# Kernel tuning notes

Hardware: AMD Instinct MI355X
Metric: run time of the kernel (lower is better)

## Reference

```python
import jax, jax.numpy as jnp
import numpy as np

N = 512          # nodes per sample (num_nodes)
B = 8            # batch size (samples)
H = 64           # hidden_dim
SPARSITY = 0.1
K = int(SPARSITY * N * (N - 1))  # edges kept per sample (fixed, static)


def setup_inputs() -> dict:
    key = jax.random.key(0)
    ks = jax.random.split(key, 8)

    def lin(k, fi, fo):
        w = jax.random.normal(k, (fi, fo), jnp.float32) / np.sqrt(fi).astype(np.float32)
        b = jnp.zeros((fo,), jnp.float32)
        return w, b

    w_emb, b_emb = lin(ks[0], 1, H)
    w_proj, b_proj = lin(ks[1], H, H)
    w1, b1 = lin(ks[2], 2 * H, H)
    w2, b2 = lin(ks[3], H, H // 2)
    w3, b3 = lin(ks[4], H // 2, 1)
    x = jax.random.uniform(ks[5], (B * N, 1), jnp.float32)  # abundances >= 0
    batch = jnp.repeat(jnp.arange(B, dtype=jnp.int32), N)   # [B*N]
    return dict(x=x, w_emb=w_emb, b_emb=b_emb, w_proj=w_proj, b_proj=b_proj,
                w1=w1, b1=b1, w2=w2, b2=b2, w3=w3, b3=b3, batch=batch)


def reference(x, w_emb, b_emb, w_proj, b_proj, w1, b1, w2, b2, w3, b3, batch):
    # node embedding + projection (dropout is eval-mode no-op)
    emb = jax.nn.relu(x @ w_emb + b_emb) @ w_proj + b_proj     # [B*N, H]
    emb = emb.reshape(B, N, H)
    # first pairwise-MLP layer: cat([e_i, e_j]) @ w1 == e_i @ w1a + e_j @ w1b
    w1a, w1b = w1[:H], w1[H:]
    ai = emb @ w1a                                            # [B, N, H]
    aj = emb @ w1b                                            # [B, N, H]
    h1 = jax.nn.relu(ai[:, :, None, :] + aj[:, None, :, :] + b1)   # [B, N, N, H]
    h2 = jax.nn.relu(jnp.einsum('bijh,hk->bijk', h1, w2) + b2)     # [B, N, N, H/2]
    probs = jax.nn.sigmoid(jnp.einsum('bijk,ko->bij', h2, w3) + b3[0])  # [B, N, N]
    probs = 0.5 * (probs + jnp.swapaxes(probs, 1, 2))          # symmetrize
    probs = probs * (1.0 - jnp.eye(N, dtype=probs.dtype))      # mask diagonal
    flat = probs.reshape(B, N * N)
    _, idx = jax.lax.top_k(flat, K)                            # [B, K]
    idx = jnp.sort(idx, axis=-1)                               # row-major order (dense_to_sparse)
    vals = jnp.take_along_axis(flat, idx, axis=-1)             # [B, K]
    offsets = (jnp.arange(B) * N)[:, None]                     # node offset per sample
    rows = idx // N + offsets
    cols = idx % N + offsets
    edge_index = jnp.stack([rows.reshape(-1), cols.reshape(-1)], axis=0)  # [2, B*K]
    edge_weights = vals.reshape(-1)                            # [B*K]
    adj = jnp.zeros((B, N * N), flat.dtype).at[jnp.arange(B)[:, None], idx].set(vals)
    adj = adj.reshape(B, N, N)                                 # sparse adjacency per sample
    return edge_index, edge_weights, adj
```

## Files before the change

kernel.cpp:

```cpp
#include <hip/hip_runtime.h>

#define NV 512
#define BV 8
#define KSEL 26163
#define NNv (NV*NV)
#define BKv (BV*KSEL)
#define CAPB 32768
#define DELTA 1e-4f

typedef unsigned int u32;
typedef __attribute__((ext_vector_type(8))) _Float16 f16x8;
typedef __attribute__((ext_vector_type(4))) float f32x4;

__global__ void __launch_bounds__(256) k_embed(
    const float* __restrict__ x, const float* __restrict__ w_emb,
    const float* __restrict__ b_emb, const float* __restrict__ w_proj,
    const float* __restrict__ b_proj, const float* __restrict__ w1,
    const float* __restrict__ b1,
    float* __restrict__ ai, float* __restrict__ aj, float* __restrict__ ajb) {
    __shared__ float sh[4][64];
    __shared__ float se[4][64];
    const int c = threadIdx.x;
    const int lr = threadIdx.y;
    const int row = blockIdx.x * 4 + lr;
    const float xv = x[row];
    sh[lr][c] = fmaxf(fmaf(xv, w_emb[c], b_emb[c]), 0.f);
    __syncthreads();
    float e = 0.f;
#pragma unroll
    for (int h = 0; h < 64; ++h) e = fmaf(sh[lr][h], w_proj[h * 64 + c], e);
    se[lr][c] = e + b_proj[c];
    __syncthreads();
    float a0 = 0.f, a1 = 0.f;
#pragma unroll
    for (int h = 0; h < 64; ++h) {
        const float ev = se[lr][h];
        a0 = fmaf(ev, w1[h * 64 + c], a0);
        a1 = fmaf(ev, w1[(64 + h) * 64 + c], a1);
    }
    ai[row * 64 + c] = a0;
    aj[row * 64 + c] = a1;
    ajb[row * 64 + c] = a1 + b1[c];
}

__global__ void __launch_bounds__(256) k_pairs_mfma(
    const float* __restrict__ ai, const float* __restrict__ ajb,
    const float* __restrict__ w2, const float* __restrict__ b2,
    const float* __restrict__ w3, const float* __restrict__ b3,
    float* __restrict__ probs) {
    __shared__ float s_ai[2048];
    const int tid = threadIdx.x;
    const int b = blockIdx.z;
    const int i0 = blockIdx.y << 5;
    const int j0 = blockIdx.x << 6;
    {
        const int r = tid >> 3, c8 = (tid & 7) << 3;
        const float* src = &ai[(((b << 9) + i0 + r) << 6) + c8];
        *(float4*)&s_ai[(r << 6) + c8]     = *(const float4*)&src[0];
        *(float4*)&s_ai[(r << 6) + c8 + 4] = *(const float4*)&src[4];
    }
    const int lane = tid & 63;
    const int wv = tid >> 6;
    const int lp = lane & 15;
    const int lg = lane >> 4;
    const int j = j0 + (wv << 4) + lp;

    float ajr[2][8];
    {
        const float* base = &ajb[(((b << 9) + j) << 6) + (lg << 3)];
        *(float4*)&ajr[0][0] = *(const float4*)&base[0];
        *(float4*)&ajr[0][4] = *(const float4*)&base[4];
        *(float4*)&ajr[1][0] = *(const float4*)&base[32];
        *(float4*)&ajr[1][4] = *(const float4*)&base[36];
    }
    f16x8 Ah[2][2], Al[2][2];
#pragma unroll
    for (int kt = 0; kt < 2; ++kt)
#pragma unroll
        for (int ch = 0; ch < 2; ++ch)
#pragma unroll
            for (int e = 0; e < 8; ++e) {
                const float wv2 = w2[((ch << 5) + (lg << 3) + e) * 32 + (kt << 4) + lp];
                const _Float16 wh = (_Float16)wv2;
                Ah[kt][ch][e] = wh;
                Al[kt][ch][e] = (_Float16)((wv2 - (float)wh) * 2048.0f);
            }
    float b2r[2][4], w3r[2][4];
#pragma unroll
    for (int kt = 0; kt < 2; ++kt)
#pragma unroll
        for (int r = 0; r < 4; ++r) {
            b2r[kt][r] = b2[(kt << 4) + (lg << 2) + r];
            w3r[kt][r] = w3[(kt << 4) + (lg << 2) + r];
        }
    const float b3v = b3[0];
    __syncthreads();

    for (int i = 0; i < 32; ++i) {
        float ar[2][8];
        const float* arow = &s_ai[(i << 6) + (lg << 3)];
        *(float4*)&ar[0][0] = *(const float4*)&arow[0];
        *(float4*)&ar[0][4] = *(const float4*)&arow[4];
        *(float4*)&ar[1][0] = *(const float4*)&arow[32];
        *(float4*)&ar[1][4] = *(const float4*)&arow[36];
        f16x8 Bh0, Bh1, Bl0, Bl1;
#pragma unroll
        for (int e = 0; e < 8; ++e) {
            const float t0 = fmaxf(ar[0][e] + ajr[0][e], 0.f) * 256.0f;
            const float t1 = fmaxf(ar[1][e] + ajr[1][e], 0.f) * 256.0f;
            const _Float16 h0 = (_Float16)t0;
            const _Float16 h1 = (_Float16)t1;
            Bh0[e] = h0; Bl0[e] = (_Float16)((t0 - (float)h0) * 2048.0f);
            Bh1[e] = h1; Bl1[e] = (_Float16)((t1 - (float)h1) * 2048.0f);
        }
        f32x4 am0 = {0.f,0.f,0.f,0.f}, am1 = {0.f,0.f,0.f,0.f};
        f32x4 ac0 = {0.f,0.f,0.f,0.f}, ac1 = {0.f,0.f,0.f,0.f};
        am0 = __builtin_amdgcn_mfma_f32_16x16x32_f16(Ah[0][0], Bh0, am0, 0, 0, 0);
        am0 = __builtin_amdgcn_mfma_f32_16x16x32_f16(Ah[0][1], Bh1, am0, 0, 0, 0);
        ac0 = __builtin_amdgcn_mfma_f32_16x16x32_f16(Ah[0][0], Bl0, ac0, 0, 0, 0);
        ac0 = __builtin_amdgcn_mfma_f32_16x16x32_f16(Ah[0][1], Bl1, ac0, 0, 0, 0);
        ac0 = __builtin_amdgcn_mfma_f32_16x16x32_f16(Al[0][0], Bh0, ac0, 0, 0, 0);
        ac0 = __builtin_amdgcn_mfma_f32_16x16x32_f16(Al[0][1], Bh1, ac0, 0, 0, 0);
        am1 = __builtin_amdgcn_mfma_f32_16x16x32_f16(Ah[1][0], Bh0, am1, 0, 0, 0);
        am1 = __builtin_amdgcn_mfma_f32_16x16x32_f16(Ah[1][1], Bh1, am1, 0, 0, 0);
        ac1 = __builtin_amdgcn_mfma_f32_16x16x32_f16(Ah[1][0], Bl0, ac1, 0, 0, 0);
        ac1 = __builtin_amdgcn_mfma_f32_16x16x32_f16(Ah[1][1], Bl1, ac1, 0, 0, 0);
        ac1 = __builtin_amdgcn_mfma_f32_16x16x32_f16(Al[1][0], Bh0, ac1, 0, 0, 0);
        ac1 = __builtin_amdgcn_mfma_f32_16x16x32_f16(Al[1][1], Bh1, ac1, 0, 0, 0);
        float s = 0.f;
#pragma unroll
        for (int r = 0; r < 4; ++r) {
            const float h2 = fmaf(ac0[r], 1.9073486328125e-6f, am0[r] * 0.00390625f);
            s = fmaf(fmaxf(h2 + b2r[0][r], 0.f), w3r[0][r], s);
        }
#pragma unroll
        for (int r = 0; r < 4; ++r) {
            const float h2 = fmaf(ac1[r], 1.9073486328125e-6f, am1[r] * 0.00390625f);
            s = fmaf(fmaxf(h2 + b2r[1][r], 0.f), w3r[1][r], s);
        }
        s += __shfl_xor(s, 16);
        s += __shfl_xor(s, 32);
        const float p = 1.f / (1.f + expf(-(s + b3v)));
        if (lane < 16) probs[(((b << 9) + i0 + i) << 9) + j] = p;
    }
}

__global__ void k_sym(float* __restrict__ P) {
    const int b = blockIdx.y;
    int rem = blockIdx.x, ta = 0;
    while (rem >= 16 - ta) { rem -= 16 - ta; ++ta; }
    const int tb = ta + rem;
    const int r  = threadIdx.x >> 3;
    const int c4 = (threadIdx.x & 7) << 2;
    const int i = (ta << 5) + r;
    const int j = (tb << 5) + c4;
    float* Pb = P + b * NNv;
    float4 a = *(const float4*)&Pb[(i << 9) + j];
    float t0 = Pb[((j + 0) << 9) + i];
    float t1 = Pb[((j + 1) << 9) + i];
    float t2 = Pb[((j + 2) << 9) + i];
    float t3 = Pb[((j + 3) << 9) + i];
    __syncthreads();
    float4 o;
    o.x = (i == j + 0) ? 0.f : 0.5f * (a.x + t0);
    o.y = (i == j + 1) ? 0.f : 0.5f * (a.y + t1);
    o.z = (i == j + 2) ? 0.f : 0.5f * (a.z + t2);
    o.w = (i == j + 3) ? 0.f : 0.5f * (a.w + t3);
    *(float4*)&Pb[(i << 9) + j] = o;
    Pb[((j + 0) << 9) + i] = o.x;
    Pb[((j + 1) << 9) + i] = o.y;
    Pb[((j + 2) << 9) + i] = o.z;
    Pb[((j + 3) << 9) + i] = o.w;
}

template <int PASS>
__global__ void k_hist(const float* __restrict__ probs,
                       const u32* __restrict__ prefix, u32* __restrict__ hist) {
    __shared__ u32 lh[1024];
    const int t = threadIdx.x;
    lh[t] = 0u; lh[256 + t] = 0u; lh[512 + t] = 0u; lh[768 + t] = 0u;
    __syncthreads();
    const int b = blockIdx.y;
    u32 pref = 0u;
    if constexpr (PASS > 0) pref = prefix[b];
    const float* Pb = probs + b * NNv;
    const int base = blockIdx.x * 4096 + t;
    const int rep = (t & 3) << 8;
#pragma unroll
    for (int e = 0; e < 16; ++e) {
        const u32 key = __float_as_uint(Pb[base + e * 256]);
        bool ok = true;
        if constexpr (PASS > 0) ok = ((key >> (32 - 8 * PASS)) == pref);
        if (ok) atomicAdd(&lh[rep + ((key >> (24 - 8 * PASS)) & 255u)], 1u);
    }
    __syncthreads();
    const u32 sum = lh[t] + lh[256 + t] + lh[512 + t] + lh[768 + t];
    if (sum) atomicAdd(&hist[b * 256 + t], sum);
}

template <int FIRST>
__global__ void k_selp(const u32* __restrict__ hist, u32* __restrict__ prefix,
                       u32* __restrict__ rem) {
    __shared__ u32 s[256];
    const int b = blockIdx.x, t = threadIdx.x;
    s[t] = hist[b * 256 + t];
    __syncthreads();
    for (int off = 1; off < 256; off <<= 1) {
        const u32 v = (t + off < 256) ? s[t + off] : 0u;
        __syncthreads();
        s[t] += v;
        __syncthreads();
    }
    const u32 remv = FIRST ? (u32)KSEL : rem[b];
    const u32 above = (t < 255) ? s[t + 1] : 0u;
    if (s[t] >= remv && above < remv) {
        rem[b] = remv - above;
        prefix[b] = (prefix[b] << 8) | (u32)t;
    }
}

__global__ void k_thr(const u32* __restrict__ prefix, float* __restrict__ thr) {
    const int b = threadIdx.x;
    if (b >= 8) return;
    const u32 p24 = prefix[b];
    thr[b]     = __uint_as_float(p24 << 8) - 2.f * DELTA;
    thr[8 + b] = __uint_as_float((p24 + 1u) << 8) + 2.f * DELTA;
}

__global__ void __launch_bounds__(256) k_band(
    const float* __restrict__ P, const float* __restrict__ thr,
    u32* __restrict__ C_in, u32* __restrict__ bandCnt, u32* __restrict__ bandIdx) {
    __shared__ u32 lidx[1024];
    __shared__ u32 lcnt, lhi, gbase;
    const int b = blockIdx.y, blk = blockIdx.x, t = threadIdx.x;
    if (t == 0) { lcnt = 0u; lhi = 0u; }
    __syncthreads();
    const float Tlo = thr[b], Thi = thr[8 + b];
    const int fi0 = blk * 1024 + t * 4;
    const float4 v = *(const float4*)&P[b * NNv + fi0];
    const float vv[4] = {v.x, v.y, v.z, v.w};
    u32 hc = 0;
#pragma unroll
    for (int q = 0; q < 4; ++q) {
        const float xq = vv[q];
        if (xq > Thi) ++hc;
        else if (xq >= Tlo) { u32 p = atomicAdd(&lcnt, 1u); lidx[p] = (u32)(fi0 + q); }
    }
    if (hc) atomicAdd(&lhi, hc);
    __syncthreads();
    if (t == 0) {
        if (lhi) atomicAdd(&C_in[b], lhi);
        gbase = lcnt ? atomicAdd(&bandCnt[b], lcnt) : 0u;
    }
    __syncthreads();
    for (u32 p = t; p < lcnt; p += 256) {
        const u32 g = gbase + p;
        if (g < (u32)CAPB) bandIdx[b * CAPB + g] = lidx[p];
    }
}

__device__ __forceinline__ float exact_p(const float* __restrict__ rai,
                                         const float* __restrict__ raj,
                                         const float* __restrict__ s_w2,
                                         const float* __restrict__ s_b1,
                                         const float* __restrict__ s_b2,
                                         const float* __restrict__ s_w3,
                                         float b3v) {
    float acc[32];
#pragma unroll
    for (int k = 0; k < 32; ++k) acc[k] = 0.f;
#pragma unroll 1
    for (int h0 = 0; h0 < 64; h0 += 16) {
        float A[16], J[16];
#pragma unroll
        for (int q = 0; q < 4; ++q) {
            *(float4*)&A[q * 4] = *(const float4*)&rai[h0 + q * 4];
            *(float4*)&J[q * 4] = *(const float4*)&raj[h0 + q * 4];
        }
#pragma unroll
        for (int hh = 0; hh < 16; ++hh) {
            const float tv = fmaxf((A[hh] + J[hh]) + s_b1[h0 + hh], 0.f);
#pragma unroll
            for (int k = 0; k < 32; ++k) acc[k] = fmaf(tv, s_w2[(h0 + hh) * 32 + k], acc[k]);
        }
    }
    float d = 0.f;
#pragma unroll
    for (int k = 0; k < 32; ++k) d = fmaf(fmaxf(acc[k] + s_b2[k], 0.f), s_w3[k], d);
    return 1.f / (1.f + expf(-(d + b3v)));
}

__global__ void __launch_bounds__(256) k_band_exact(
    const float* __restrict__ ai, const float* __restrict__ aj,
    const float* __restrict__ b1, const float* __restrict__ w2,
    const float* __restrict__ b2, const float* __restrict__ w3,
    const float* __restrict__ b3, const u32* __restrict__ bandCnt,
    const u32* __restrict__ bandIdx, float* __restrict__ bandVal) {
    __shared__ float s_w2[2048];
    __shared__ float s_b1[64], s_b2[32], s_w3[32];
    const int b = blockIdx.y, t = threadIdx.x;
    {
        const int o = t * 8;
        *(float4*)&s_w2[o]     = *(const float4*)&w2[o];
        *(float4*)&s_w2[o + 4] = *(const float4*)&w2[o + 4];
        if (t < 64) s_b1[t] = b1[t];
        if (t < 32) { s_b2[t] = b2[t]; s_w3[t] = w3[t]; }
    }
    __syncthreads();
    const u32 nb = min(bandCnt[b], (u32)CAPB);
    const float b3v = b3[0];
    for (u32 e = blockIdx.x * 256 + t; e < nb; e += 2048) {
        const u32 idx = bandIdx[b * CAPB + e];
        const int i = (int)(idx >> 9), j = (int)(idx & 511u);
        const float* ri  = &ai[(((b << 9) + i)) << 6];
        const float* rj  = &aj[(((b << 9) + j)) << 6];
        const float* rj2 = &ai[(((b << 9) + j)) << 6];
        const float* ri2 = &aj[(((b << 9) + i)) << 6];
        const float p1 = exact_p(ri, rj, s_w2, s_b1, s_b2, s_w3, b3v);
        const float p2 = exact_p(rj2, ri2, s_w2, s_b1, s_b2, s_w3, b3v);
        bandVal[b * CAPB + e] = 0.5f * (p1 + p2);
    }
}

__global__ void __launch_bounds__(256) k_band_select(
    const u32* __restrict__ bandCnt, const u32* __restrict__ C_in,
    const u32* __restrict__ bandIdx, const float* __restrict__ bandVal,
    u32* __restrict__ bitmap) {
    __shared__ u32 red[256];
    __shared__ u32 tie[8192];
    __shared__ u32 tieCnt;
    const int b = blockIdx.x, t = threadIdx.x;
    const u32 nb = min(bandCnt[b], (u32)CAPB);
    const u32 Kp = (u32)KSEL - C_in[b];
    const u32* vb = (const u32*)(bandVal + b * CAPB);
    const u32* ib = bandIdx + b * CAPB;
    u32* bm = bitmap + b * 8192;
    u32 mn = 0xFFFFFFFFu, mx = 0u;
    for (u32 e = t; e < nb; e += 256) { const u32 v = vb[e]; mn = min(mn, v); mx = max(mx, v); }
    red[t] = mn; __syncthreads();
    for (int s = 128; s > 0; s >>= 1) { if (t < s) red[t] = min(red[t], red[t + s]); __syncthreads(); }
    const u32 glo = red[0]; __syncthreads();
    red[t] = mx; __syncthreads();
    for (int s = 128; s > 0; s >>= 1) { if (t < s) red[t] = max(red[t], red[t + s]); __syncthreads(); }
    const u32 ghi = red[0]; __syncthreads();
    u32 lo = glo, hi = ghi;
    while (lo < hi) {
        const u32 mid = lo + ((hi - lo) >> 1);
        u32 c = 0;
        for (u32 e = t; e < nb; e += 256) c += (vb[e] > mid);
        red[t] = c; __syncthreads();
        for (int s = 128; s > 0; s >>= 1) { if (t < s) red[t] += red[t + s]; __syncthreads(); }
        const u32 tot = red[0]; __syncthreads();
        if (tot >= Kp) lo = mid + 1; else hi = mid;
    }
    const u32 Tx = lo;
    if (t == 0) tieCnt = 0u;
    __syncthreads();
    u32 c = 0;
    for (u32 e = t; e < nb; e += 256) {
        const u32 v = vb[e];
        if (v > Tx) {
            ++c;
            const u32 idx = ib[e];
            atomicOr(&bm[idx >> 5], 1u << (idx & 31u));
        } else if (v == Tx) {
            const u32 p = atomicAdd(&tieCnt, 1u);
            if (p < 8192u) tie[p] = ib[e];
        }
    }
    red[t] = c; __syncthreads();
    for (int s = 128; s > 0; s >>= 1) { if (t < s) red[t] += red[t + s]; __syncthreads(); }
    const u32 Ap = red[0]; __syncthreads();
    const u32 Rp = Kp - Ap;
    const u32 E = min(tieCnt, 8192u);
    for (u32 e = t; e < E; e += 256) {
        const u32 my = tie[e];
        u32 r = 0;
        for (u32 m = 0; m < E; ++m) r += (tie[m] < my);
        if (r < Rp) atomicOr(&bm[my >> 5], 1u << (my & 31u));
    }
}

__global__ void k_count(const float* __restrict__ P, const float* __restrict__ thr,
                        const u32* __restrict__ bitmap, u32* __restrict__ bgt) {
    __shared__ u32 sg[256];
    const int b = blockIdx.y, blk = blockIdx.x, t = threadIdx.x;
    const float Thi = thr[8 + b];
    const int fi0 = blk * 1024 + t * 4;
    const float4 v = *(const float4*)&P[b * NNv + fi0];
    const float vv[4] = {v.x, v.y, v.z, v.w};
    const u32 w = bitmap[b * 8192 + (fi0 >> 5)];
    const u32 sh = (u32)(fi0 & 31);
    u32 cnt = 0;
#pragma unroll
    for (int q = 0; q < 4; ++q) cnt += (vv[q] > Thi) || ((w >> (sh + q)) & 1u);
    sg[t] = cnt;
    __syncthreads();
    for (int s = 128; s > 0; s >>= 1) { if (t < s) sg[t] += sg[t + s]; __syncthreads(); }
    if (t == 0) bgt[b * 256 + blk] = sg[0];
}

__global__ void k_scan1(const u32* __restrict__ bgt, u32* __restrict__ goff) {
    __shared__ u32 sg[256];
    const int b = blockIdx.x, t = threadIdx.x;
    const u32 g = bgt[b * 256 + t];
    sg[t] = g;
    __syncthreads();
    for (int off = 1; off < 256; off <<= 1) {
        const u32 a = (t >= off) ? sg[t - off] : 0u;
        __syncthreads();
        sg[t] += a;
        __syncthreads();
    }
    goff[b * 256 + t] = sg[t] - g;
}

__global__ void k_write(const float* __restrict__ P, const float* __restrict__ thr,
                        const u32* __restrict__ bitmap, const u32* __restrict__ goff,
                        float* __restrict__ out) {
    __shared__ u32 sg[256];
    const int b = blockIdx.y, blk = blockIdx.x, t = threadIdx.x;
    const float Thi = thr[8 + b];
    const int pbase = b * NNv;
    const int fi0 = blk * 1024 + t * 4;
    const float4 v = *(const float4*)&P[pbase + fi0];
    const float vv[4] = {v.x, v.y, v.z, v.w};
    const u32 w = bitmap[b * 8192 + (fi0 >> 5)];
    const u32 sh = (u32)(fi0 & 31);
    bool sel[4];
    u32 cnt = 0;
#pragma unroll
    for (int q = 0; q < 4; ++q) {
        sel[q] = (vv[q] > Thi) || ((w >> (sh + q)) & 1u);
        cnt += sel[q];
    }
    sg[t] = cnt;
    __syncthreads();
    for (int off = 1; off < 256; off <<= 1) {
        const u32 a = (t >= off) ? sg[t - off] : 0u;
        __syncthreads();
        sg[t] += a;
        __syncthreads();
    }
    u32 pos = goff[b * 256 + blk] + sg[t] - cnt;
#pragma unroll
    for (int q = 0; q < 4; ++q) {
        if (sel[q]) {
            if (pos < (u32)KSEL) {
                const int g = b * KSEL + (int)pos;
                const int fi = fi0 + q;
                const int row = fi >> 9, col = fi & 511;
                out[g]           = (float)(row + (b << 9));
                out[BKv + g]     = (float)(col + (b << 9));
                out[2 * BKv + g] = vv[q];
                out[3 * BKv + pbase + fi] = vv[q];
            }
            ++pos;
        }
    }
}

extern "C" void kernel_launch(void* const* d_in, const int* in_sizes, int n_in,
                              void* d_out, int out_size, void* d_ws, size_t ws_size,
                              hipStream_t stream) {
    const float* x      = (const float*)d_in[0];
    const float* w_emb  = (const float*)d_in[1];
    const float* b_emb  = (const float*)d_in[2];
    const float* w_proj = (const float*)d_in[3];
    const float* b_proj = (const float*)d_in[4];
    const float* w1     = (const float*)d_in[5];
    const float* b1     = (const float*)d_in[6];
    const float* w2     = (const float*)d_in[7];
    const float* b2     = (const float*)d_in[8];
    const float* w3     = (const float*)d_in[9];
    const float* b3     = (const float*)d_in[10];
    (void)in_sizes; (void)n_in; (void)ws_size;

    char* ws = (char*)d_ws;
    float* ai      = (float*)(ws);
    float* aj      = (float*)(ws + 1048576);
    float* ajb     = (float*)(ws + 2097152);
    float* probs   = (float*)(ws + 3145728);
    u32*   bandIdx = (u32*)  (ws + 11534336);
    float* bandVal = (float*)(ws + 12582912);
    const size_t SOFF = 13631488;
    u32*   hist0   = (u32*)  (ws + SOFF);
    u32*   hist1   = (u32*)  (ws + SOFF + 8192);
    u32*   hist2   = (u32*)  (ws + SOFF + 16384);
    u32*   prefix  = (u32*)  (ws + SOFF + 24576);
    u32*   rem     = (u32*)  (ws + SOFF + 24608);
    float* thr     = (float*)(ws + SOFF + 24640);
    u32*   C_in    = (u32*)  (ws + SOFF + 24704);
    u32*   bandCnt = (u32*)  (ws + SOFF + 24736);
    u32*   bitmap  = (u32*)  (ws + SOFF + 24832);
    u32*   bgt     = (u32*)  (ws + SOFF + 286976);
    u32*   goff    = (u32*)  (ws + SOFF + 295168);

    float* out = (float*)d_out;

    hipMemsetAsync(d_out, 0, (size_t)out_size * sizeof(float), stream);
    hipMemsetAsync(ws + SOFF, 0, 286976, stream);

    k_embed<<<1024, dim3(64, 4, 1), 0, stream>>>(x, w_emb, b_emb, w_proj, b_proj, w1, b1, ai, aj, ajb);
    k_pairs_mfma<<<dim3(8, 16, 8), 256, 0, stream>>>(ai, ajb, w2, b2, w3, b3, probs);
    k_sym<<<dim3(136, 8), 256, 0, stream>>>(probs);
    k_hist<0><<<dim3(64, 8), 256, 0, stream>>>(probs, prefix, hist0);
    k_selp<1><<<8, 256, 0, stream>>>(hist0, prefix, rem);
    k_hist<1><<<dim3(64, 8), 256, 0, stream>>>(probs, prefix, hist1);
    k_selp<0><<<8, 256, 0, stream>>>(hist1, prefix, rem);
    k_hist<2><<<dim3(64, 8), 256, 0, stream>>>(probs, prefix, hist2);
    k_selp<0><<<8, 256, 0, stream>>>(hist2, prefix, rem);
    k_thr<<<1, 64, 0, stream>>>(prefix, thr);
    k_band<<<dim3(256, 8), 256, 0, stream>>>(probs, thr, C_in, bandCnt, bandIdx);
    k_band_exact<<<dim3(8, 8), 256, 0, stream>>>(ai, aj, b1, w2, b2, w3, b3, bandCnt, bandIdx, bandVal);
    k_band_select<<<8, 256, 0, stream>>>(bandCnt, C_in, bandIdx, bandVal, bitmap);
    k_count<<<dim3(256, 8), 256, 0, stream>>>(probs, thr, bitmap, bgt);
    k_scan1<<<8, 256, 0, stream>>>(bgt, goff);
    k_write<<<dim3(256, 8), 256, 0, stream>>>(probs, thr, bitmap, goff, out);
}
```

Before: 203.1 us.

## Fuse pair MLP with symmetrization and first histogram; shorten radix select pipeline

The pairwise MLP now computes each upper-triangular 32x32 tile pair in both directions inside one block, then symmetrizes, masks the diagonal and builds the top-byte histogram in shared memory. This removes the separate k_sym pass and the first histogram pass over probs. The three 8-bit radix passes are replaced by one 8-bit pass plus one 16-bit global histogram. The per-block count kernel is dropped; k_band and k_band_select now fill the per-block counts directly. Packed f32 ops, pre-scaled inputs and a mask-based hi/lo split trim the fp16 conversion work, at the cost of a 2 MB histogram memset and extra atomics.

```diff
diff --git a/kernel.cpp b/kernel.cpp
--- a/kernel.cpp
+++ b/kernel.cpp
@@ -9,15 +9,31 @@
 #define DELTA 1e-4f
 
 typedef unsigned int u32;
+typedef __attribute__((ext_vector_type(2))) float f32x2;
+typedef __attribute__((ext_vector_type(4))) float f32x4;
+typedef __attribute__((ext_vector_type(4))) u32 u32x4;
 typedef __attribute__((ext_vector_type(8))) _Float16 f16x8;
-typedef __attribute__((ext_vector_type(4))) float f32x4;
+
+__device__ __forceinline__ f32x2 pk_add(f32x2 a, f32x2 b) {
+    f32x2 d; asm("v_pk_add_f32 %0, %1, %2" : "=v"(d) : "v"(a), "v"(b)); return d;
+}
+__device__ __forceinline__ f32x2 pk_mul(f32x2 a, f32x2 b) {
+    f32x2 d; asm("v_pk_mul_f32 %0, %1, %2" : "=v"(d) : "v"(a), "v"(b)); return d;
+}
+__device__ __forceinline__ f32x2 pk_fma(f32x2 a, f32x2 b, f32x2 c) {
+    f32x2 d; asm("v_pk_fma_f32 %0, %1, %2, %3" : "=v"(d) : "v"(a), "v"(b), "v"(c)); return d;
+}
+__device__ __forceinline__ u32 pkrtz(float a, float b) {
+    u32 d; asm("v_cvt_pkrtz_f16_f32 %0, %1, %2" : "=v"(d) : "v"(a), "v"(b)); return d;
+}
 
 __global__ void __launch_bounds__(256) k_embed(
     const float* __restrict__ x, const float* __restrict__ w_emb,
     const float* __restrict__ b_emb, const float* __restrict__ w_proj,
     const float* __restrict__ b_proj, const float* __restrict__ w1,
     const float* __restrict__ b1,
-    float* __restrict__ ai, float* __restrict__ aj, float* __restrict__ ajb) {
+    float* __restrict__ ai, float* __restrict__ aj,
+    float* __restrict__ ai256, float* __restrict__ ajb256) {
     __shared__ float sh[4][64];
     __shared__ float se[4][64];
     const int c = threadIdx.x;
@@ -40,34 +56,46 @@
     }
     ai[row * 64 + c] = a0;
     aj[row * 64 + c] = a1;
-    ajb[row * 64 + c] = a1 + b1[c];
-}
-
-__global__ void __launch_bounds__(256) k_pairs_mfma(
-    const float* __restrict__ ai, const float* __restrict__ ajb,
+    ai256[row * 64 + c] = a0 * 256.0f;
+    ajb256[row * 64 + c] = (a1 + b1[c]) * 256.0f;
+}
+
+__global__ void __launch_bounds__(256) k_pairs_sym(
+    const float* __restrict__ ai256, const float* __restrict__ ajb256,
     const float* __restrict__ w2, const float* __restrict__ b2,
     const float* __restrict__ w3, const float* __restrict__ b3,
-    float* __restrict__ probs) {
-    __shared__ float s_ai[2048];
+    float* __restrict__ probs, u32* __restrict__ hist8) {
+    __shared__ float sI[2048];
+    __shared__ float sJ[2048];
+    __shared__ float sp1[32 * 36];
+    __shared__ float sp2[32 * 36];
+    __shared__ u32 lh[1024];
     const int tid = threadIdx.x;
-    const int b = blockIdx.z;
-    const int i0 = blockIdx.y << 5;
-    const int j0 = blockIdx.x << 6;
+    const int b = blockIdx.y;
+    int remb = blockIdx.x, ta = 0;
+    while (remb >= 16 - ta) { remb -= 16 - ta; ++ta; }
+    const int tb = ta + remb;
+    const int i0 = ta << 5, j0 = tb << 5;
     {
         const int r = tid >> 3, c8 = (tid & 7) << 3;
-        const float* src = &ai[(((b << 9) + i0 + r) << 6) + c8];
-        *(float4*)&s_ai[(r << 6) + c8]     = *(const float4*)&src[0];
-        *(float4*)&s_ai[(r << 6) + c8 + 4] = *(const float4*)&src[4];
+        const float* srcI = &ai256[(((b << 9) + i0 + r) << 6) + c8];
+        *(float4*)&sI[(r << 6) + c8]     = *(const float4*)&srcI[0];
+        *(float4*)&sI[(r << 6) + c8 + 4] = *(const float4*)&srcI[4];
+        const float* srcJ = &ai256[(((b << 9) + j0 + r) << 6) + c8];
+        *(float4*)&sJ[(r << 6) + c8]     = *(const float4*)&srcJ[0];
+        *(float4*)&sJ[(r << 6) + c8 + 4] = *(const float4*)&srcJ[4];
+        lh[tid] = 0; lh[256 + tid] = 0; lh[512 + tid] = 0; lh[768 + tid] = 0;
     }
     const int lane = tid & 63;
-    const int wv = tid >> 6;
-    const int lp = lane & 15;
-    const int lg = lane >> 4;
-    const int j = j0 + (wv << 4) + lp;
-
-    float ajr[2][8];
+    const int lp = lane & 15, lg = lane >> 4;
+    const int wave = tid >> 6;
+    const int dir = wave >> 1, wc = wave & 1;
+    const int colb = (wc << 4) + lp;
+    const int colg = (dir ? i0 : j0) + colb;
+
+    alignas(16) float ajr[2][8];
     {
-        const float* base = &ajb[(((b << 9) + j) << 6) + (lg << 3)];
+        const float* base = &ajb256[(((b << 9) + colg) << 6) + (lg << 3)];
         *(float4*)&ajr[0][0] = *(const float4*)&base[0];
         *(float4*)&ajr[0][4] = *(const float4*)&base[4];
         *(float4*)&ajr[1][0] = *(const float4*)&base[32];
@@ -85,34 +113,51 @@
                 Ah[kt][ch][e] = wh;
                 Al[kt][ch][e] = (_Float16)((wv2 - (float)wh) * 2048.0f);
             }
-    float b2r[2][4], w3r[2][4];
+    float b2f[2][4], w3f[2][4];
 #pragma unroll
     for (int kt = 0; kt < 2; ++kt)
 #pragma unroll
         for (int r = 0; r < 4; ++r) {
-            b2r[kt][r] = b2[(kt << 4) + (lg << 2) + r];
-            w3r[kt][r] = w3[(kt << 4) + (lg << 2) + r];
+            b2f[kt][r] = b2[(kt << 4) + (lg << 2) + r] * 256.0f;
+            w3f[kt][r] = w3[(kt << 4) + (lg << 2) + r] * 0.00390625f;
         }
     const float b3v = b3[0];
     __syncthreads();
 
-    for (int i = 0; i < 32; ++i) {
-        float ar[2][8];
-        const float* arow = &s_ai[(i << 6) + (lg << 3)];
-        *(float4*)&ar[0][0] = *(const float4*)&arow[0];
-        *(float4*)&ar[0][4] = *(const float4*)&arow[4];
-        *(float4*)&ar[1][0] = *(const float4*)&arow[32];
-        *(float4*)&ar[1][4] = *(const float4*)&arow[36];
-        f16x8 Bh0, Bh1, Bl0, Bl1;
-#pragma unroll
-        for (int e = 0; e < 8; ++e) {
-            const float t0 = fmaxf(ar[0][e] + ajr[0][e], 0.f) * 256.0f;
-            const float t1 = fmaxf(ar[1][e] + ajr[1][e], 0.f) * 256.0f;
-            const _Float16 h0 = (_Float16)t0;
-            const _Float16 h1 = (_Float16)t1;
-            Bh0[e] = h0; Bl0[e] = (_Float16)((t0 - (float)h0) * 2048.0f);
-            Bh1[e] = h1; Bl1[e] = (_Float16)((t1 - (float)h1) * 2048.0f);
-        }
+    const float* __restrict__ sA = dir ? sJ : sI;
+    float* __restrict__ spO = dir ? sp2 : sp1;
+    const f32x2 C2048 = {2048.f, 2048.f};
+    const f32x2 CN2048 = {-2048.f, -2048.f};
+
+    for (int r = 0; r < 32; ++r) {
+        alignas(16) float ar[2][8];
+        *(float4*)&ar[0][0] = *(const float4*)&sA[(r << 6) + (lg << 3)];
+        *(float4*)&ar[0][4] = *(const float4*)&sA[(r << 6) + (lg << 3) + 4];
+        *(float4*)&ar[1][0] = *(const float4*)&sA[(r << 6) + 32 + (lg << 3)];
+        *(float4*)&ar[1][4] = *(const float4*)&sA[(r << 6) + 32 + (lg << 3) + 4];
+        alignas(16) u32 hw[2][4], lw[2][4];
+#pragma unroll
+        for (int c = 0; c < 2; ++c)
+#pragma unroll
+            for (int e2 = 0; e2 < 4; ++e2) {
+                const f32x2 a2 = *(const f32x2*)&ar[c][e2 * 2];
+                const f32x2 j2 = *(const f32x2*)&ajr[c][e2 * 2];
+                const f32x2 t2 = pk_add(a2, j2);
+                const float u0 = fmaxf(t2[0], 0.f);
+                const float u1 = fmaxf(t2[1], 0.f);
+                hw[c][e2] = pkrtz(u0, u1);
+                f32x2 u2; u2[0] = u0; u2[1] = u1;
+                f32x2 hif;
+                hif[0] = __uint_as_float(__float_as_uint(u0) & 0xFFFFE000u);
+                hif[1] = __uint_as_float(__float_as_uint(u1) & 0xFFFFE000u);
+                const f32x2 tm = pk_mul(u2, C2048);
+                const f32x2 lo = pk_fma(hif, CN2048, tm);
+                lw[c][e2] = pkrtz(lo[0], lo[1]);
+            }
+        const f16x8 Bh0 = __builtin_bit_cast(f16x8, *(u32x4*)&hw[0][0]);
+        const f16x8 Bh1 = __builtin_bit_cast(f16x8, *(u32x4*)&hw[1][0]);
+        const f16x8 Bl0 = __builtin_bit_cast(f16x8, *(u32x4*)&lw[0][0]);
+        const f16x8 Bl1 = __builtin_bit_cast(f16x8, *(u32x4*)&lw[1][0]);
         f32x4 am0 = {0.f,0.f,0.f,0.f}, am1 = {0.f,0.f,0.f,0.f};
         f32x4 ac0 = {0.f,0.f,0.f,0.f}, ac1 = {0.f,0.f,0.f,0.f};
         am0 = __builtin_amdgcn_mfma_f32_16x16x32_f16(Ah[0][0], Bh0, am0, 0, 0, 0);
@@ -129,81 +174,98 @@
         ac1 = __builtin_amdgcn_mfma_f32_16x16x32_f16(Al[1][1], Bh1, ac1, 0, 0, 0);
         float s = 0.f;
 #pragma unroll
-        for (int r = 0; r < 4; ++r) {
-            const float h2 = fmaf(ac0[r], 1.9073486328125e-6f, am0[r] * 0.00390625f);
-            s = fmaf(fmaxf(h2 + b2r[0][r], 0.f), w3r[0][r], s);
-        }
-#pragma unroll
-        for (int r = 0; r < 4; ++r) {
-            const float h2 = fmaf(ac1[r], 1.9073486328125e-6f, am1[r] * 0.00390625f);
-            s = fmaf(fmaxf(h2 + b2r[1][r], 0.f), w3r[1][r], s);
+        for (int q = 0; q < 4; ++q) {
+            const float amc = fmaf(ac0[q], 4.8828125e-4f, am0[q]);
+            s = fmaf(fmaxf(amc + b2f[0][q], 0.f), w3f[0][q], s);
+        }
+#pragma unroll
+        for (int q = 0; q < 4; ++q) {
+            const float amc = fmaf(ac1[q], 4.8828125e-4f, am1[q]);
+            s = fmaf(fmaxf(amc + b2f[1][q], 0.f), w3f[1][q], s);
         }
         s += __shfl_xor(s, 16);
         s += __shfl_xor(s, 32);
-        const float p = 1.f / (1.f + expf(-(s + b3v)));
-        if (lane < 16) probs[(((b << 9) + i0 + i) << 9) + j] = p;
-    }
-}
-
-__global__ void k_sym(float* __restrict__ P) {
+        const float p = 1.f / (1.f + __expf(-(s + b3v)));
+        if (lane < 16) {
+            if (dir == 0) spO[r * 36 + colb] = p;
+            else          spO[colb * 36 + r] = p;
+        }
+    }
+    __syncthreads();
+
+    {
+        const int pr = tid >> 3;
+        const int pc = (tid & 7) << 2;
+        const int rep = (tid & 3) << 8;
+        const bool diag = (ta == tb);
+        float4 vo;
+        float vq[4];
+#pragma unroll
+        for (int q = 0; q < 4; ++q) {
+            float v = 0.5f * (sp1[pr * 36 + pc + q] + sp2[pr * 36 + pc + q]);
+            if (diag && pr == pc + q) v = 0.f;
+            vq[q] = v;
+            atomicAdd(&lh[rep + (__float_as_uint(v) >> 24)], diag ? 1u : 2u);
+        }
+        vo.x = vq[0]; vo.y = vq[1]; vo.z = vq[2]; vo.w = vq[3];
+        *(float4*)&probs[(((b << 9) + i0 + pr) << 9) + j0 + pc] = vo;
+        if (!diag) {
+            const int qr = tid >> 3;
+            const int qc = (tid & 7) << 2;
+            float4 w4;
+            w4.x = 0.5f * (sp1[(qc + 0) * 36 + qr] + sp2[(qc + 0) * 36 + qr]);
+            w4.y = 0.5f * (sp1[(qc + 1) * 36 + qr] + sp2[(qc + 1) * 36 + qr]);
+            w4.z = 0.5f * (sp1[(qc + 2) * 36 + qr] + sp2[(qc + 2) * 36 + qr]);
+            w4.w = 0.5f * (sp1[(qc + 3) * 36 + qr] + sp2[(qc + 3) * 36 + qr]);
+            *(float4*)&probs[(((b << 9) + j0 + qr) << 9) + i0 + qc] = w4;
+        }
+    }
+    __syncthreads();
+    const u32 sum = lh[tid] + lh[256 + tid] + lh[512 + tid] + lh[768 + tid];
+    if (sum) atomicAdd(&hist8[b * 256 + tid], sum);
+}
+
+__global__ void k_selp8(const u32* __restrict__ hist8, u32* __restrict__ c8,
+                        u32* __restrict__ rem1) {
+    __shared__ u32 s[256];
+    const int b = blockIdx.x, t = threadIdx.x;
+    s[t] = hist8[b * 256 + t];
+    __syncthreads();
+    for (int off = 1; off < 256; off <<= 1) {
+        const u32 v = (t + off < 256) ? s[t + off] : 0u;
+        __syncthreads();
+        s[t] += v;
+        __syncthreads();
+    }
+    const u32 above = (t < 255) ? s[t + 1] : 0u;
+    if (s[t] >= (u32)KSEL && above < (u32)KSEL) {
+        c8[b] = (u32)t;
+        rem1[b] = (u32)KSEL - above;
+    }
+}
+
+__global__ void k_hist16(const float* __restrict__ probs,
+                         const u32* __restrict__ c8, u32* __restrict__ hist16) {
     const int b = blockIdx.y;
-    int rem = blockIdx.x, ta = 0;
-    while (rem >= 16 - ta) { rem -= 16 - ta; ++ta; }
-    const int tb = ta + rem;
-    const int r  = threadIdx.x >> 3;
-    const int c4 = (threadIdx.x & 7) << 2;
-    const int i = (ta << 5) + r;
-    const int j = (tb << 5) + c4;
-    float* Pb = P + b * NNv;
-    float4 a = *(const float4*)&Pb[(i << 9) + j];
-    float t0 = Pb[((j + 0) << 9) + i];
-    float t1 = Pb[((j + 1) << 9) + i];
-    float t2 = Pb[((j + 2) << 9) + i];
-    float t3 = Pb[((j + 3) << 9) + i];
-    __syncthreads();
-    float4 o;
-    o.x = (i == j + 0) ? 0.f : 0.5f * (a.x + t0);
-    o.y = (i == j + 1) ? 0.f : 0.5f * (a.y + t1);
-    o.z = (i == j + 2) ? 0.f : 0.5f * (a.z + t2);
-    o.w = (i == j + 3) ? 0.f : 0.5f * (a.w + t3);
-    *(float4*)&Pb[(i << 9) + j] = o;
-    Pb[((j + 0) << 9) + i] = o.x;
-    Pb[((j + 1) << 9) + i] = o.y;
-    Pb[((j + 2) << 9) + i] = o.z;
-    Pb[((j + 3) << 9) + i] = o.w;
-}
-
-template <int PASS>
-__global__ void k_hist(const float* __restrict__ probs,
-                       const u32* __restrict__ prefix, u32* __restrict__ hist) {
-    __shared__ u32 lh[1024];
-    const int t = threadIdx.x;
-    lh[t] = 0u; lh[256 + t] = 0u; lh[512 + t] = 0u; lh[768 + t] = 0u;
-    __syncthreads();
-    const int b = blockIdx.y;
-    u32 pref = 0u;
-    if constexpr (PASS > 0) pref = prefix[b];
+    const u32 sel = c8[b];
     const float* Pb = probs + b * NNv;
-    const int base = blockIdx.x * 4096 + t;
-    const int rep = (t & 3) << 8;
+    const int base = blockIdx.x * 4096 + threadIdx.x;
+    u32* H = hist16 + b * 65536;
 #pragma unroll
     for (int e = 0; e < 16; ++e) {
         const u32 key = __float_as_uint(Pb[base + e * 256]);
-        bool ok = true;
-        if constexpr (PASS > 0) ok = ((key >> (32 - 8 * PASS)) == pref);
-        if (ok) atomicAdd(&lh[rep + ((key >> (24 - 8 * PASS)) & 255u)], 1u);
-    }
-    __syncthreads();
-    const u32 sum = lh[t] + lh[256 + t] + lh[512 + t] + lh[768 + t];
-    if (sum) atomicAdd(&hist[b * 256 + t], sum);
-}
-
-template <int FIRST>
-__global__ void k_selp(const u32* __restrict__ hist, u32* __restrict__ prefix,
-                       u32* __restrict__ rem) {
+        if ((key >> 24) == sel) atomicAdd(&H[(key >> 8) & 0xFFFFu], 1u);
+    }
+}
+
+__global__ void k_sel16(const u32* __restrict__ hist16, const u32* __restrict__ c8,
+                        const u32* __restrict__ rem1, float* __restrict__ thr) {
     __shared__ u32 s[256];
     const int b = blockIdx.x, t = threadIdx.x;
-    s[t] = hist[b * 256 + t];
+    const u32* H = hist16 + b * 65536;
+    u32 sum = 0;
+    for (int k = 0; k < 256; ++k) sum += H[t * 256 + k];
+    s[t] = sum;
     __syncthreads();
     for (int off = 1; off < 256; off <<= 1) {
         const u32 v = (t + off < 256) ? s[t + off] : 0u;
@@ -211,25 +273,26 @@
         s[t] += v;
         __syncthreads();
     }
-    const u32 remv = FIRST ? (u32)KSEL : rem[b];
+    const u32 remv = rem1[b];
     const u32 above = (t < 255) ? s[t + 1] : 0u;
     if (s[t] >= remv && above < remv) {
-        rem[b] = remv - above;
-        prefix[b] = (prefix[b] << 8) | (u32)t;
-    }
-}
-
-__global__ void k_thr(const u32* __restrict__ prefix, float* __restrict__ thr) {
-    const int b = threadIdx.x;
-    if (b >= 8) return;
-    const u32 p24 = prefix[b];
-    thr[b]     = __uint_as_float(p24 << 8) - 2.f * DELTA;
-    thr[8 + b] = __uint_as_float((p24 + 1u) << 8) + 2.f * DELTA;
+        u32 cum = above;
+        for (int c = 255; c >= 0; --c) {
+            cum += H[t * 256 + c];
+            if (cum >= remv) {
+                const u32 p24 = (c8[b] << 16) | (u32)(t * 256 + c);
+                thr[b]     = __uint_as_float(p24 << 8) - 2.f * DELTA;
+                thr[8 + b] = __uint_as_float((p24 + 1u) << 8) + 2.f * DELTA;
+                break;
+            }
+        }
+    }
 }
 
 __global__ void __launch_bounds__(256) k_band(
     const float* __restrict__ P, const float* __restrict__ thr,
-    u32* __restrict__ C_in, u32* __restrict__ bandCnt, u32* __restrict__ bandIdx) {
+    u32* __restrict__ C_in, u32* __restrict__ bandCnt, u32* __restrict__ bandIdx,
+    u32* __restrict__ bgt) {
     __shared__ u32 lidx[1024];
     __shared__ u32 lcnt, lhi, gbase;
     const int b = blockIdx.y, blk = blockIdx.x, t = threadIdx.x;
@@ -249,6 +312,7 @@
     if (hc) atomicAdd(&lhi, hc);
     __syncthreads();
     if (t == 0) {
+        bgt[b * 256 + blk] = lhi;
         if (lhi) atomicAdd(&C_in[b], lhi);
         gbase = lcnt ? atomicAdd(&bandCnt[b], lcnt) : 0u;
     }
@@ -325,7 +389,7 @@
 __global__ void __launch_bounds__(256) k_band_select(
     const u32* __restrict__ bandCnt, const u32* __restrict__ C_in,
     const u32* __restrict__ bandIdx, const float* __restrict__ bandVal,
-    u32* __restrict__ bitmap) {
+    u32* __restrict__ bitmap, u32* __restrict__ bgt) {
     __shared__ u32 red[256];
     __shared__ u32 tie[8192];
     __shared__ u32 tieCnt;
@@ -363,6 +427,7 @@
             ++c;
             const u32 idx = ib[e];
             atomicOr(&bm[idx >> 5], 1u << (idx & 31u));
+            atomicAdd(&bgt[b * 256 + (idx >> 10)], 1u);
         } else if (v == Tx) {
             const u32 p = atomicAdd(&tieCnt, 1u);
             if (p < 8192u) tie[p] = ib[e];
@@ -377,27 +442,11 @@
         const u32 my = tie[e];
         u32 r = 0;
         for (u32 m = 0; m < E; ++m) r += (tie[m] < my);
-        if (r < Rp) atomicOr(&bm[my >> 5], 1u << (my & 31u));
-    }
-}
-
-__global__ void k_count(const float* __restrict__ P, const float* __restrict__ thr,
-                        const u32* __restrict__ bitmap, u32* __restrict__ bgt) {
-    __shared__ u32 sg[256];
-    const int b = blockIdx.y, blk = blockIdx.x, t = threadIdx.x;
-    const float Thi = thr[8 + b];
-    const int fi0 = blk * 1024 + t * 4;
-    const float4 v = *(const float4*)&P[b * NNv + fi0];
-    const float vv[4] = {v.x, v.y, v.z, v.w};
-    const u32 w = bitmap[b * 8192 + (fi0 >> 5)];
-    const u32 sh = (u32)(fi0 & 31);
-    u32 cnt = 0;
-#pragma unroll
-    for (int q = 0; q < 4; ++q) cnt += (vv[q] > Thi) || ((w >> (sh + q)) & 1u);
-    sg[t] = cnt;
-    __syncthreads();
-    for (int s = 128; s > 0; s >>= 1) { if (t < s) sg[t] += sg[t + s]; __syncthreads(); }
-    if (t == 0) bgt[b * 256 + blk] = sg[0];
+        if (r < Rp) {
+            atomicOr(&bm[my >> 5], 1u << (my & 31u));
+            atomicAdd(&bgt[b * 256 + (my >> 10)], 1u);
+        }
+    }
 }
 
 __global__ void k_scan1(const u32* __restrict__ bgt, u32* __restrict__ goff) {
@@ -479,42 +528,40 @@
     char* ws = (char*)d_ws;
     float* ai      = (float*)(ws);
     float* aj      = (float*)(ws + 1048576);
-    float* ajb     = (float*)(ws + 2097152);
-    float* probs   = (float*)(ws + 3145728);
-    u32*   bandIdx = (u32*)  (ws + 11534336);
-    float* bandVal = (float*)(ws + 12582912);
-    const size_t SOFF = 13631488;
-    u32*   hist0   = (u32*)  (ws + SOFF);
-    u32*   hist1   = (u32*)  (ws + SOFF + 8192);
-    u32*   hist2   = (u32*)  (ws + SOFF + 16384);
-    u32*   prefix  = (u32*)  (ws + SOFF + 24576);
-    u32*   rem     = (u32*)  (ws + SOFF + 24608);
-    float* thr     = (float*)(ws + SOFF + 24640);
-    u32*   C_in    = (u32*)  (ws + SOFF + 24704);
-    u32*   bandCnt = (u32*)  (ws + SOFF + 24736);
-    u32*   bitmap  = (u32*)  (ws + SOFF + 24832);
-    u32*   bgt     = (u32*)  (ws + SOFF + 286976);
-    u32*   goff    = (u32*)  (ws + SOFF + 295168);
+    float* ai256   = (float*)(ws + 2097152);
+    float* ajb256  = (float*)(ws + 3145728);
+    u32*   hist16  = (u32*)  (ws + 2097152);
+    float* probs   = (float*)(ws + 4194304);
+    u32*   bandIdx = (u32*)  (ws + 12582912);
+    float* bandVal = (float*)(ws + 13631488);
+    const size_t SOFF = 14680064;
+    u32*   hist8   = (u32*)  (ws + SOFF);
+    u32*   c8      = (u32*)  (ws + SOFF + 8192);
+    u32*   rem1    = (u32*)  (ws + SOFF + 8224);
+    float* thr     = (float*)(ws + SOFF + 8256);
+    u32*   C_in    = (u32*)  (ws + SOFF + 8320);
+    u32*   bandCnt = (u32*)  (ws + SOFF + 8352);
+    u32*   bitmap  = (u32*)  (ws + SOFF + 8448);
+    u32*   bgt     = (u32*)  (ws + SOFF + 270592);
+    u32*   goff    = (u32*)  (ws + SOFF + 278784);
 
     float* out = (float*)d_out;
 
     hipMemsetAsync(d_out, 0, (size_t)out_size * sizeof(float), stream);
-    hipMemsetAsync(ws + SOFF, 0, 286976, stream);
-
-    k_embed<<<1024, dim3(64, 4, 1), 0, stream>>>(x, w_emb, b_emb, w_proj, b_proj, w1, b1, ai, aj, ajb);
-    k_pairs_mfma<<<dim3(8, 16, 8), 256, 0, stream>>>(ai, ajb, w2, b2, w3, b3, probs);
-    k_sym<<<dim3(136, 8), 256, 0, stream>>>(probs);
-    k_hist<0><<<dim3(64, 8), 256, 0, stream>>>(probs, prefix, hist0);
-    k_selp<1><<<8, 256, 0, stream>>>(hist0, prefix, rem);
-    k_hist<1><<<dim3(64, 8), 256, 0, stream>>>(probs, prefix, hist1);
-    k_selp<0><<<8, 256, 0, stream>>>(hist1, prefix, rem);
-    k_hist<2><<<dim3(64, 8), 256, 0, stream>>>(probs, prefix, hist2);
-    k_selp<0><<<8, 256, 0, stream>>>(hist2, prefix, rem);
-    k_thr<<<1, 64, 0, stream>>>(prefix, thr);
-    k_band<<<dim3(256, 8), 256, 0, stream>>>(probs, thr, C_in, bandCnt, bandIdx);
-    k_band_exact<<<dim3(8, 8), 256, 0, stream>>>(ai, aj, b1, w2, b2, w3, b3, bandCnt, bandIdx, bandVal);
-    k_band_select<<<8, 256, 0, stream>>>(bandCnt, C_in, bandIdx, bandVal, bitmap);
-    k_count<<<dim3(256, 8), 256, 0, stream>>>(probs, thr, bitmap, bgt);
+    hipMemsetAsync(ws + SOFF, 0, 270592, stream);
+
+    k_embed<<<1024, dim3(64, 4, 1), 0, stream>>>(x, w_emb, b_emb, w_proj, b_proj,
+                                                 w1, b1, ai, aj, ai256, ajb256);
+    k_pairs_sym<<<dim3(136, 8), 256, 0, stream>>>(ai256, ajb256, w2, b2, w3, b3,
+                                                  probs, hist8);
+    k_selp8<<<8, 256, 0, stream>>>(hist8, c8, rem1);
+    hipMemsetAsync(hist16, 0, 2097152, stream);
+    k_hist16<<<dim3(64, 8), 256, 0, stream>>>(probs, c8, hist16);
+    k_sel16<<<8, 256, 0, stream>>>(hist16, c8, rem1, thr);
+    k_band<<<dim3(256, 8), 256, 0, stream>>>(probs, thr, C_in, bandCnt, bandIdx, bgt);
+    k_band_exact<<<dim3(8, 8), 256, 0, stream>>>(ai, aj, b1, w2, b2, w3, b3,
+                                                 bandCnt, bandIdx, bandVal);
+    k_band_select<<<8, 256, 0, stream>>>(bandCnt, C_in, bandIdx, bandVal, bitmap, bgt);
     k_scan1<<<8, 256, 0, stream>>>(bgt, goff);
     k_write<<<dim3(256, 8), 256, 0, stream>>>(probs, thr, bitmap, goff, out);
 }
```

After: 295.8 us. 45.7% more time.
